# Optimization experiments

Hardware: AMD Instinct MI355X
Metric: run time of the kernel (lower is better)

## Reference

```python
import jax, jax.numpy as jnp
import numpy as np

B, T, D, H = 2, 2048, 1024, 16
DH = D // H

def setup_inputs() -> dict:
    key = jax.random.key(0)
    ks = jax.random.split(key, 5)
    scale = 1.0 / np.sqrt(D)
    x = jax.random.normal(ks[0], (B, T, D), dtype=jnp.float32)
    Wq = jax.random.normal(ks[1], (D, D), dtype=jnp.float32) * scale
    Wk = jax.random.normal(ks[2], (D, D), dtype=jnp.float32) * scale
    Wv = jax.random.normal(ks[3], (D, D), dtype=jnp.float32) * scale
    Wo = jax.random.normal(ks[4], (D, D), dtype=jnp.float32) * scale
    # causal mask: True means masked (matches torch masked_fill semantics)
    mask = jnp.triu(jnp.ones((T, T), dtype=bool), k=1)
    return {"x": x, "mask": mask, "Wq": Wq, "Wk": Wk, "Wv": Wv, "Wo": Wo}

def reference(x, mask, Wq, Wk, Wv, Wo):
    b, t, c = x.shape
    # projections -> [B, H, T, DH]
    def split_heads(y):
        return y.reshape(b, t, H, DH).transpose(0, 2, 1, 3)
    q = split_heads(x @ Wq)
    k = split_heads(x @ Wk)
    v = split_heads(x @ Wv)
    # scores [B, H, T, T]
    att = jnp.einsum('bhqd,bhkd->bhqk', q, k) / jnp.sqrt(jnp.float32(DH))
    att = jnp.where(mask, -jnp.inf, att)
    att = jax.nn.softmax(att, axis=-1)
    # dropout=0.0 (eval-mode determinism)
    out = jnp.einsum('bhqk,bhkd->bhqd', att, v)
    out = out.transpose(0, 2, 1, 3).reshape(b, t, c)
    return out @ Wo
```

## Files before the change

kernel.cpp:

```cpp
#include <hip/hip_runtime.h>
#include <stdint.h>

typedef unsigned short u16;
typedef unsigned int u32;
typedef __attribute__((ext_vector_type(8))) short s16x8;
typedef __attribute__((ext_vector_type(4))) float f32x4;
typedef __attribute__((ext_vector_type(8))) unsigned short u16x8;
typedef __attribute__((ext_vector_type(4))) unsigned short u16x4;

#define T_ 2048
#define D_ 1024
#define H_ 16
#define DH_ 64

#define QSCALE_LOG2E 0.18033688011112042f

#if __has_builtin(__builtin_amdgcn_exp2f)
#define EXP2(x) __builtin_amdgcn_exp2f(x)
#else
#define EXP2(x) exp2f(x)
#endif

__device__ __forceinline__ float bf2f(u16 u) {
    union { unsigned int i; float f; } x; x.i = ((unsigned int)u) << 16; return x.f;
}
__device__ __forceinline__ u16 f2bf(float f) {
    union { float f; unsigned int i; } x; x.f = f;
    unsigned int u = x.i;
    u += 0x7fffu + ((u >> 16) & 1u);
    return (u16)(u >> 16);
}
__device__ __forceinline__ u32 pack_rn(float a, float b) {
    union { float f; u32 u; } ua, ub; ua.f = a; ub.f = b;
    return ((ua.u + 0x8000u) >> 16) | ((ub.u + 0x8000u) & 0xffff0000u);
}

__device__ __forceinline__ void gload16(const u16* g, u16* l) {
    __builtin_amdgcn_global_load_lds(
        (const __attribute__((address_space(1))) void*)g,
        (__attribute__((address_space(3))) void*)l,
        16, 0, 0);
}

__global__ __launch_bounds__(256) void cvt_x_kernel(const float* __restrict__ x,
                                                    u16* __restrict__ xb) {
    int i = (blockIdx.x * 256 + threadIdx.x) * 4;
    float4 v = *(const float4*)(x + i);
    u16x4 o;
    o[0] = f2bf(v.x); o[1] = f2bf(v.y); o[2] = f2bf(v.z); o[3] = f2bf(v.w);
    *(u16x4*)(xb + i) = o;
}

__global__ __launch_bounds__(256) void transpose_w_kernel(const float* __restrict__ Wq,
                                                          const float* __restrict__ Wk,
                                                          const float* __restrict__ Wv,
                                                          const float* __restrict__ Wo,
                                                          u16* __restrict__ WT) {
    __shared__ float tile[32][33];
    int s = blockIdx.z;
    const float* W = (s == 0) ? Wq : (s == 1) ? Wk : (s == 2) ? Wv : Wo;
    int n0 = blockIdx.x * 32;
    int k0 = blockIdx.y * 32;
    int tx = threadIdx.x, ty = threadIdx.y;
    #pragma unroll
    for (int j = 0; j < 32; j += 8)
        tile[ty + j][tx] = W[(k0 + ty + j) * D_ + n0 + tx];
    __syncthreads();
    u16* dst = WT + (size_t)s * D_ * D_;
    #pragma unroll
    for (int j = 0; j < 32; j += 8)
        dst[(n0 + ty + j) * D_ + k0 + tx] = f2bf(tile[tx][ty + j]);
}

__global__ __launch_bounds__(256) void gemm_qkv(const u16* __restrict__ A,
                                                const u16* __restrict__ Bt,
                                                u16* __restrict__ Qw,
                                                u16* __restrict__ Kw,
                                                u16* __restrict__ Vw) {
    __shared__ __align__(16) u16 As[2][128 * 32];
    __shared__ __align__(16) u16 Bs[2][128 * 32];
    const int m0 = blockIdx.x * 128, n0 = blockIdx.y * 128;
    int tid = threadIdx.x;
    int w = tid >> 6, lane = tid & 63, quad = lane >> 4, l15 = lane & 15;
    int wr = w >> 1, wc = w & 1;

    int nb0 = (w << 7), nb1 = nb0 + 64;
    int c0 = nb0 + lane, c1 = nb1 + lane;
    int r0 = c0 >> 2, k0off = (c0 & 3) << 3;
    int r1 = c1 >> 2, k1off = (c1 & 3) << 3;
    const u16* Ar0 = A + (size_t)(m0 + r0) * D_ + k0off;
    const u16* Ar1 = A + (size_t)(m0 + r1) * D_ + k1off;
    const u16* Br0 = Bt + (size_t)(n0 + r0) * D_ + k0off;
    const u16* Br1 = Bt + (size_t)(n0 + r1) * D_ + k1off;

    f32x4 acc[4][4];
    #pragma unroll
    for (int mi = 0; mi < 4; ++mi)
        #pragma unroll
        for (int ni = 0; ni < 4; ++ni) acc[mi][ni] = (f32x4){0.f, 0.f, 0.f, 0.f};

    gload16(Ar0, &As[0][nb0 << 3]);
    gload16(Ar1, &As[0][nb1 << 3]);
    gload16(Br0, &Bs[0][nb0 << 3]);
    gload16(Br1, &Bs[0][nb1 << 3]);

    for (int k0 = 0; k0 < D_; k0 += 32) {
        int buf = (k0 >> 5) & 1;
        __syncthreads();
        if (k0 + 32 < D_) {
            int kn = k0 + 32;
            gload16(Ar0 + kn, &As[buf ^ 1][nb0 << 3]);
            gload16(Ar1 + kn, &As[buf ^ 1][nb1 << 3]);
            gload16(Br0 + kn, &Bs[buf ^ 1][nb0 << 3]);
            gload16(Br1 + kn, &Bs[buf ^ 1][nb1 << 3]);
        }
        s16x8 af[4], bf[4];
        #pragma unroll
        for (int mi = 0; mi < 4; ++mi)
            af[mi] = *(const s16x8*)&As[buf][((wr * 64 + mi * 16 + l15) << 5) + (quad << 3)];
        #pragma unroll
        for (int ni = 0; ni < 4; ++ni)
            bf[ni] = *(const s16x8*)&Bs[buf][((wc * 64 + ni * 16 + l15) << 5) + (quad << 3)];
        #pragma unroll
        for (int mi = 0; mi < 4; ++mi)
            #pragma unroll
            for (int ni = 0; ni < 4; ++ni)
                acc[mi][ni] = __builtin_amdgcn_mfma_f32_16x16x32_bf16(af[mi], bf[ni],
                                                                      acc[mi][ni], 0, 0, 0);
    }

    #pragma unroll
    for (int mi = 0; mi < 4; ++mi) {
        int mbase = m0 + wr * 64 + mi * 16 + quad * 4;
        #pragma unroll
        for (int ni = 0; ni < 4; ++ni) {
            int n = n0 + wc * 64 + ni * 16 + l15;
            int b = mbase >> 11, t0 = mbase & 2047;
            int sel = n >> 10, nn = n & 1023;
            int h = nn >> 6, dh = nn & 63;
            int bhidx = (b << 4) + h;
            if (sel == 0) {
                #pragma unroll
                for (int r = 0; r < 4; ++r)
                    Qw[(size_t)(bhidx * T_ + t0 + r) * DH_ + dh] =
                        f2bf(acc[mi][ni][r] * QSCALE_LOG2E);
            } else if (sel == 1) {
                #pragma unroll
                for (int r = 0; r < 4; ++r)
                    Kw[(size_t)(bhidx * T_ + t0 + r) * DH_ + dh] = f2bf(acc[mi][ni][r]);
            } else {
                uint2 pk;
                pk.x = pack_rn(acc[mi][ni][0], acc[mi][ni][1]);
                pk.y = pack_rn(acc[mi][ni][2], acc[mi][ni][3]);
                *(uint2*)(Vw + ((size_t)bhidx * DH_ + dh) * T_ + t0) = pk;
            }
        }
    }
}

__global__ __launch_bounds__(256) void gemm_out(const u16* __restrict__ A,
                                                const u16* __restrict__ Bt,
                                                float* __restrict__ Cout) {
    __shared__ __align__(16) u16 As[2][128 * 32];
    __shared__ __align__(16) u16 Bs[2][64 * 32];
    const int m0 = blockIdx.x * 128, n0 = blockIdx.y * 64;
    int tid = threadIdx.x;
    int w = tid >> 6, lane = tid & 63, quad = lane >> 4, l15 = lane & 15;

    int nbA0 = (w << 7), nbA1 = nbA0 + 64, nbB = (w << 6);
    int cA0 = nbA0 + lane, cA1 = nbA1 + lane, cB = nbB + lane;
    const u16* ArA0 = A + (size_t)(m0 + (cA0 >> 2)) * D_ + ((cA0 & 3) << 3);
    const u16* ArA1 = A + (size_t)(m0 + (cA1 >> 2)) * D_ + ((cA1 & 3) << 3);
    const u16* BrB  = Bt + (size_t)(n0 + (cB >> 2)) * D_ + ((cB & 3) << 3);

    f32x4 acc[2][4];
    #pragma unroll
    for (int mi = 0; mi < 2; ++mi)
        #pragma unroll
        for (int ni = 0; ni < 4; ++ni) acc[mi][ni] = (f32x4){0.f, 0.f, 0.f, 0.f};

    gload16(ArA0, &As[0][nbA0 << 3]);
    gload16(ArA1, &As[0][nbA1 << 3]);
    gload16(BrB,  &Bs[0][nbB << 3]);

    for (int k0 = 0; k0 < D_; k0 += 32) {
        int buf = (k0 >> 5) & 1;
        __syncthreads();
        if (k0 + 32 < D_) {
            int kn = k0 + 32;
            gload16(ArA0 + kn, &As[buf ^ 1][nbA0 << 3]);
            gload16(ArA1 + kn, &As[buf ^ 1][nbA1 << 3]);
            gload16(BrB + kn,  &Bs[buf ^ 1][nbB << 3]);
        }
        s16x8 af[2], bf[4];
        #pragma unroll
        for (int mi = 0; mi < 2; ++mi)
            af[mi] = *(const s16x8*)&As[buf][((w * 32 + mi * 16 + l15) << 5) + (quad << 3)];
        #pragma unroll
        for (int ni = 0; ni < 4; ++ni)
            bf[ni] = *(const s16x8*)&Bs[buf][((ni * 16 + l15) << 5) + (quad << 3)];
        #pragma unroll
        for (int mi = 0; mi < 2; ++mi)
            #pragma unroll
            for (int ni = 0; ni < 4; ++ni)
                acc[mi][ni] = __builtin_amdgcn_mfma_f32_16x16x32_bf16(af[mi], bf[ni],
                                                                      acc[mi][ni], 0, 0, 0);
    }

    #pragma unroll
    for (int mi = 0; mi < 2; ++mi) {
        int mbase = m0 + w * 32 + mi * 16 + quad * 4;
        #pragma unroll
        for (int ni = 0; ni < 4; ++ni) {
            int n = n0 + ni * 16 + l15;
            #pragma unroll
            for (int r = 0; r < 4; ++r)
                Cout[(size_t)(mbase + r) * D_ + n] = acc[mi][ni][r];
        }
    }
}

__global__ __launch_bounds__(256) void attn_mfma_kernel(const u16* __restrict__ Qg,
                                                        const u16* __restrict__ Kg,
                                                        const u16* __restrict__ Vt,
                                                        u16* __restrict__ att) {
    __shared__ __align__(16) u16 Kbuf[2][64 * 64];
    __shared__ __align__(16) u16 Vbuf[2][64 * 64];
    __shared__ __align__(16) u16 Ps[4][2][16][72];

    int bx = (int)gridDim.x - 1 - (int)blockIdx.x;
    int bh = blockIdx.y;
    int tid = threadIdx.x;
    int w = tid >> 6, lane = tid & 63, quad = lane >> 4, l15 = lane & 15;
    int q0 = bx * 128;
    int qA = q0 + 16 * w;
    int qB = q0 + 64 + 16 * w;

    const u16* Qb = Qg + (size_t)bh * T_ * DH_;
    const u16* Kb = Kg + (size_t)bh * T_ * DH_;
    const u16* Vb = Vt + (size_t)bh * DH_ * T_;

    s16x8 qa0 = *(const s16x8*)(Qb + (size_t)(qA + l15) * DH_ + quad * 8);
    s16x8 qa1 = *(const s16x8*)(Qb + (size_t)(qA + l15) * DH_ + quad * 8 + 32);
    s16x8 qc0 = *(const s16x8*)(Qb + (size_t)(qB + l15) * DH_ + quad * 8);
    s16x8 qc1 = *(const s16x8*)(Qb + (size_t)(qB + l15) * DH_ + quad * 8 + 32);

    int nb0 = (w << 7), nb1 = nb0 + 64;
    int n0c = nb0 + lane, n1c = nb1 + lane;
    int r0 = n0c >> 3, c0s = n0c & 7, g0 = (r0 << 3) + (c0s ^ (r0 & 7));
    int r1 = n1c >> 3, c1s = n1c & 7, g1 = (r1 << 3) + (c1s ^ (r1 & 7));

    gload16(Kb + (g0 << 3), &Kbuf[0][nb0 << 3]);
    gload16(Kb + (g1 << 3), &Kbuf[0][nb1 << 3]);
    gload16(Vb + (size_t)r0 * T_ + ((g0 & 7) << 3), &Vbuf[0][nb0 << 3]);
    gload16(Vb + (size_t)r1 * T_ + ((g1 & 7) << 3), &Vbuf[0][nb1 << 3]);

    f32x4 oA[4] = {{0.f,0.f,0.f,0.f},{0.f,0.f,0.f,0.f},{0.f,0.f,0.f,0.f},{0.f,0.f,0.f,0.f}};
    f32x4 oB[4] = {{0.f,0.f,0.f,0.f},{0.f,0.f,0.f,0.f},{0.f,0.f,0.f,0.f},{0.f,0.f,0.f,0.f}};
    float lA = 0.f, lB = 0.f;

    int ktmax = 2 * bx + 1;
    for (int kt = 0; kt <= ktmax; ++kt) {
        int buf = kt & 1;
        __syncthreads();

        if (kt < ktmax) {
            int kb2 = (kt + 1) << 6;
            const u16* Ktile = Kb + (size_t)kb2 * DH_;
            gload16(Ktile + (g0 << 3), &Kbuf[buf ^ 1][nb0 << 3]);
            gload16(Ktile + (g1 << 3), &Kbuf[buf ^ 1][nb1 << 3]);
            gload16(Vb + (size_t)r0 * T_ + kb2 + ((g0 & 7) << 3), &Vbuf[buf ^ 1][nb0 << 3]);
            gload16(Vb + (size_t)r1 * T_ + kb2 + ((g1 & 7) << 3), &Vbuf[buf ^ 1][nb1 << 3]);
        }

        f32x4 sA[4], sB[4];
        #pragma unroll
        for (int g = 0; g < 4; ++g) {
            int r = (g << 4) + l15;
            int cc = quad ^ (r & 7);
            s16x8 ka0 = *(const s16x8*)&Kbuf[buf][((r << 3) + cc) << 3];
            s16x8 ka1 = *(const s16x8*)&Kbuf[buf][((r << 3) + (cc ^ 4)) << 3];
            f32x4 z = {0.f, 0.f, 0.f, 0.f};
            sA[g] = __builtin_amdgcn_mfma_f32_16x16x32_bf16(ka0, qa0, z, 0, 0, 0);
            sA[g] = __builtin_amdgcn_mfma_f32_16x16x32_bf16(ka1, qa1, sA[g], 0, 0, 0);
            sB[g] = __builtin_amdgcn_mfma_f32_16x16x32_bf16(ka0, qc0, z, 0, 0, 0);
            sB[g] = __builtin_amdgcn_mfma_f32_16x16x32_bf16(ka1, qc1, sB[g], 0, 0, 0);
        }

        if (kt >= ktmax - 1) {
            int rA = q0 + 16 * w + l15 - (kt << 6);
            #pragma unroll
            for (int g = 0; g < 4; ++g)
                #pragma unroll
                for (int r = 0; r < 4; ++r)
                    if ((g << 4) + (quad << 2) + r > rA) sA[g][r] = -INFINITY;
        }
        if (kt == ktmax) {
            int rB = 16 * w + l15;
            #pragma unroll
            for (int g = 0; g < 4; ++g)
                #pragma unroll
                for (int r = 0; r < 4; ++r)
                    if ((g << 4) + (quad << 2) + r > rB) sB[g][r] = -INFINITY;
        }

        #pragma unroll
        for (int g = 0; g < 4; ++g)
            #pragma unroll
            for (int r = 0; r < 4; ++r) {
                float pA = EXP2(sA[g][r]); sA[g][r] = pA; lA += pA;
                float pB = EXP2(sB[g][r]); sB[g][r] = pB; lB += pB;
            }

        #pragma unroll
        for (int g = 0; g < 4; ++g) {
            uint2 pkA, pkB;
            pkA.x = pack_rn(sA[g][0], sA[g][1]); pkA.y = pack_rn(sA[g][2], sA[g][3]);
            pkB.x = pack_rn(sB[g][0], sB[g][1]); pkB.y = pack_rn(sB[g][2], sB[g][3]);
            *(uint2*)&Ps[w][0][l15][g * 16 + quad * 4] = pkA;
            *(uint2*)&Ps[w][1][l15][g * 16 + quad * 4] = pkB;
        }
        s16x8 pa0 = *(const s16x8*)&Ps[w][0][l15][quad * 8];
        s16x8 pa1 = *(const s16x8*)&Ps[w][0][l15][quad * 8 + 32];
        s16x8 pc0 = *(const s16x8*)&Ps[w][1][l15][quad * 8];
        s16x8 pc1 = *(const s16x8*)&Ps[w][1][l15][quad * 8 + 32];

        #pragma unroll
        for (int g = 0; g < 4; ++g) {
            int r = (g << 4) + l15;
            int cc = quad ^ (r & 7);
            s16x8 va0 = *(const s16x8*)&Vbuf[buf][((r << 3) + cc) << 3];
            s16x8 va1 = *(const s16x8*)&Vbuf[buf][((r << 3) + (cc ^ 4)) << 3];
            oA[g] = __builtin_amdgcn_mfma_f32_16x16x32_bf16(va0, pa0, oA[g], 0, 0, 0);
            oA[g] = __builtin_amdgcn_mfma_f32_16x16x32_bf16(va1, pa1, oA[g], 0, 0, 0);
            oB[g] = __builtin_amdgcn_mfma_f32_16x16x32_bf16(va0, pc0, oB[g], 0, 0, 0);
            oB[g] = __builtin_amdgcn_mfma_f32_16x16x32_bf16(va1, pc1, oB[g], 0, 0, 0);
        }
    }

    lA += __shfl_xor(lA, 16); lA += __shfl_xor(lA, 32);
    lB += __shfl_xor(lB, 16); lB += __shfl_xor(lB, 32);
    float invA = 1.f / lA, invB = 1.f / lB;
    int b = bh >> 4, h = bh & 15;
    u16* dstA = att + (size_t)(b * T_ + qA + l15) * D_ + (h << 6);
    u16* dstB = att + (size_t)(b * T_ + qB + l15) * D_ + (h << 6);
    #pragma unroll
    for (int g = 0; g < 4; ++g) {
        uint2 pk;
        pk.x = (u32)f2bf(oA[g][0] * invA) | ((u32)f2bf(oA[g][1] * invA) << 16);
        pk.y = (u32)f2bf(oA[g][2] * invA) | ((u32)f2bf(oA[g][3] * invA) << 16);
        *(uint2*)(dstA + (g << 4) + (quad << 2)) = pk;
        pk.x = (u32)f2bf(oB[g][0] * invB) | ((u32)f2bf(oB[g][1] * invB) << 16);
        pk.y = (u32)f2bf(oB[g][2] * invB) | ((u32)f2bf(oB[g][3] * invB) << 16);
        *(uint2*)(dstB + (g << 4) + (quad << 2)) = pk;
    }
}

extern "C" void kernel_launch(void* const* d_in, const int* in_sizes, int n_in,
                              void* d_out, int out_size, void* d_ws, size_t ws_size,
                              hipStream_t stream) {
    const float* x  = (const float*)d_in[0];
    const float* Wq = (const float*)d_in[2];
    const float* Wk = (const float*)d_in[3];
    const float* Wv = (const float*)d_in[4];
    const float* Wo = (const float*)d_in[5];
    float* out = (float*)d_out;

    char* ws = (char*)d_ws;
    u16* xb  = (u16*)(ws);
    u16* WT  = (u16*)(ws + (8ull  << 20));
    u16* Qw  = (u16*)(ws + (16ull << 20));
    u16* Kw  = (u16*)(ws + (24ull << 20));
    u16* Vw  = (u16*)(ws + (32ull << 20));
    u16* att = (u16*)(ws + (40ull << 20));

    cvt_x_kernel<<<dim3(4096), dim3(256), 0, stream>>>(x, xb);
    transpose_w_kernel<<<dim3(32, 32, 4), dim3(32, 8), 0, stream>>>(Wq, Wk, Wv, Wo, WT);
    gemm_qkv<<<dim3(32, 24), dim3(256), 0, stream>>>(xb, WT, Qw, Kw, Vw);
    attn_mfma_kernel<<<dim3(16, 32), dim3(256), 0, stream>>>(Qw, Kw, Vw, att);
    gemm_out<<<dim3(32, 16), dim3(256), 0, stream>>>(att, WT + 3ull * 1048576ull, out);
}
```

Baseline: 209.4 us.

## Split causal attention along KV into chunks and add a reduction kernel

The attention kernel now launches a flat 1280-block grid. Each block handles a 128-query tile and a chunk of up to 8 KV tiles, so long causal rows are spread across several blocks, and the grid is mapped so each XCD gets four heads. Partial unnormalized outputs (bf16) and row sums are written to workspace, and a new reduce kernel sums the chunks and normalizes. This targets load imbalance and low occupancy from the causal triangle, at the cost of an extra launch, extra global traffic, and bf16 rounding of the partials. Combining chunks without a running max is valid only because the kernel already skips max subtraction.

```diff
diff --git a/kernel.cpp b/kernel.cpp
--- a/kernel.cpp
+++ b/kernel.cpp
@@ -223,16 +223,28 @@
 __global__ __launch_bounds__(256) void attn_mfma_kernel(const u16* __restrict__ Qg,
                                                         const u16* __restrict__ Kg,
                                                         const u16* __restrict__ Vt,
-                                                        u16* __restrict__ att) {
+                                                        u16* __restrict__ Opart,
+                                                        float* __restrict__ lpart) {
     __shared__ __align__(16) u16 Kbuf[2][64 * 64];
     __shared__ __align__(16) u16 Vbuf[2][64 * 64];
     __shared__ __align__(16) u16 Ps[4][2][16][72];
 
-    int bx = (int)gridDim.x - 1 - (int)blockIdx.x;
-    int bh = blockIdx.y;
+    int blk = blockIdx.x;
+    int xcd = blk & 7, slot = blk >> 3;
+    int bh = (xcd << 2) + (slot / 40);
+    int x  = slot % 40;
+    int BX, c;
+    if (x < 4)       { BX = x;                    c = 0; }
+    else if (x < 12) { BX = 4 + ((x - 4) >> 1);   c = (x - 4) & 1; }
+    else if (x < 24) { BX = 8 + (x - 12) / 3;     c = (x - 12) % 3; }
+    else             { BX = 12 + ((x - 24) >> 2); c = (x - 24) & 3; }
+    int kstart = c << 3;
+    int ktm = 2 * BX + 1;
+    int kend = min(kstart + 8, ktm + 1);
+
     int tid = threadIdx.x;
     int w = tid >> 6, lane = tid & 63, quad = lane >> 4, l15 = lane & 15;
-    int q0 = bx * 128;
+    int q0 = BX << 7;
     int qA = q0 + 16 * w;
     int qB = q0 + 64 + 16 * w;
 
@@ -250,21 +262,24 @@
     int r0 = n0c >> 3, c0s = n0c & 7, g0 = (r0 << 3) + (c0s ^ (r0 & 7));
     int r1 = n1c >> 3, c1s = n1c & 7, g1 = (r1 << 3) + (c1s ^ (r1 & 7));
 
-    gload16(Kb + (g0 << 3), &Kbuf[0][nb0 << 3]);
-    gload16(Kb + (g1 << 3), &Kbuf[0][nb1 << 3]);
-    gload16(Vb + (size_t)r0 * T_ + ((g0 & 7) << 3), &Vbuf[0][nb0 << 3]);
-    gload16(Vb + (size_t)r1 * T_ + ((g1 & 7) << 3), &Vbuf[0][nb1 << 3]);
+    {
+        int kb0 = kstart << 6;
+        const u16* Ktile = Kb + (size_t)kb0 * DH_;
+        gload16(Ktile + (g0 << 3), &Kbuf[0][nb0 << 3]);
+        gload16(Ktile + (g1 << 3), &Kbuf[0][nb1 << 3]);
+        gload16(Vb + (size_t)r0 * T_ + kb0 + ((g0 & 7) << 3), &Vbuf[0][nb0 << 3]);
+        gload16(Vb + (size_t)r1 * T_ + kb0 + ((g1 & 7) << 3), &Vbuf[0][nb1 << 3]);
+    }
 
     f32x4 oA[4] = {{0.f,0.f,0.f,0.f},{0.f,0.f,0.f,0.f},{0.f,0.f,0.f,0.f},{0.f,0.f,0.f,0.f}};
     f32x4 oB[4] = {{0.f,0.f,0.f,0.f},{0.f,0.f,0.f,0.f},{0.f,0.f,0.f,0.f},{0.f,0.f,0.f,0.f}};
     float lA = 0.f, lB = 0.f;
 
-    int ktmax = 2 * bx + 1;
-    for (int kt = 0; kt <= ktmax; ++kt) {
-        int buf = kt & 1;
+    for (int kt = kstart; kt < kend; ++kt) {
+        int buf = (kt - kstart) & 1;
         __syncthreads();
 
-        if (kt < ktmax) {
+        if (kt + 1 < kend) {
             int kb2 = (kt + 1) << 6;
             const u16* Ktile = Kb + (size_t)kb2 * DH_;
             gload16(Ktile + (g0 << 3), &Kbuf[buf ^ 1][nb0 << 3]);
@@ -287,7 +302,7 @@
             sB[g] = __builtin_amdgcn_mfma_f32_16x16x32_bf16(ka1, qc1, sB[g], 0, 0, 0);
         }
 
-        if (kt >= ktmax - 1) {
+        if (kt >= ktm - 1) {
             int rA = q0 + 16 * w + l15 - (kt << 6);
             #pragma unroll
             for (int g = 0; g < 4; ++g)
@@ -295,7 +310,7 @@
                 for (int r = 0; r < 4; ++r)
                     if ((g << 4) + (quad << 2) + r > rA) sA[g][r] = -INFINITY;
         }
-        if (kt == ktmax) {
+        if (kt == ktm) {
             int rB = 16 * w + l15;
             #pragma unroll
             for (int g = 0; g < 4; ++g)
@@ -340,19 +355,63 @@
 
     lA += __shfl_xor(lA, 16); lA += __shfl_xor(lA, 32);
     lB += __shfl_xor(lB, 16); lB += __shfl_xor(lB, 32);
-    float invA = 1.f / lA, invB = 1.f / lB;
-    int b = bh >> 4, h = bh & 15;
-    u16* dstA = att + (size_t)(b * T_ + qA + l15) * D_ + (h << 6);
-    u16* dstB = att + (size_t)(b * T_ + qB + l15) * D_ + (h << 6);
+    int slotid = ((bh << 4) + BX) * 4 + c;
+    u16* dA = Opart + ((size_t)slotid * 128 + 16 * w + l15) * 64;
+    u16* dB = dA + 64 * 64;
     #pragma unroll
     for (int g = 0; g < 4; ++g) {
         uint2 pk;
-        pk.x = (u32)f2bf(oA[g][0] * invA) | ((u32)f2bf(oA[g][1] * invA) << 16);
-        pk.y = (u32)f2bf(oA[g][2] * invA) | ((u32)f2bf(oA[g][3] * invA) << 16);
-        *(uint2*)(dstA + (g << 4) + (quad << 2)) = pk;
-        pk.x = (u32)f2bf(oB[g][0] * invB) | ((u32)f2bf(oB[g][1] * invB) << 16);
-        pk.y = (u32)f2bf(oB[g][2] * invB) | ((u32)f2bf(oB[g][3] * invB) << 16);
-        *(uint2*)(dstB + (g << 4) + (quad << 2)) = pk;
+        pk.x = pack_rn(oA[g][0], oA[g][1]); pk.y = pack_rn(oA[g][2], oA[g][3]);
+        *(uint2*)(dA + (g << 4) + (quad << 2)) = pk;
+        pk.x = pack_rn(oB[g][0], oB[g][1]); pk.y = pack_rn(oB[g][2], oB[g][3]);
+        *(uint2*)(dB + (g << 4) + (quad << 2)) = pk;
+    }
+    if (quad == 0) {
+        lpart[(size_t)slotid * 128 + 16 * w + l15] = lA;
+        lpart[(size_t)slotid * 128 + 64 + 16 * w + l15] = lB;
+    }
+}
+
+__global__ __launch_bounds__(256) void reduce_attn(const u16* __restrict__ Opart,
+                                                   const float* __restrict__ lpart,
+                                                   u16* __restrict__ att) {
+    int BX = blockIdx.x, bh = blockIdx.y;
+    int nch = (BX >> 2) + 1;
+    int tid = threadIdx.x;
+    int row = tid >> 1, dh0 = (tid & 1) << 5;
+    int slotbase = ((bh << 4) + BX) << 2;
+
+    float acc[32];
+    #pragma unroll
+    for (int i = 0; i < 32; ++i) acc[i] = 0.f;
+    float l = 0.f;
+    for (int cc = 0; cc < nch; ++cc) {
+        const u16* op = Opart + ((size_t)(slotbase + cc) * 128 + row) * 64 + dh0;
+        #pragma unroll
+        for (int v = 0; v < 4; ++v) {
+            u16x8 o8 = *(const u16x8*)(op + v * 8);
+            #pragma unroll
+            for (int j = 0; j < 8; ++j) acc[v * 8 + j] += bf2f(o8[j]);
+        }
+        l += lpart[(size_t)(slotbase + cc) * 128 + row];
+    }
+    float inv = 1.f / l;
+    int b = bh >> 4, h = bh & 15;
+    int q = (BX << 7) + row;
+    u16* dst = att + ((size_t)(b * T_) + q) * D_ + (h << 6) + dh0;
+    #pragma unroll
+    for (int v = 0; v < 2; ++v) {
+        u16x8 o8;
+        #pragma unroll
+        for (int j = 0; j < 8; ++j) o8[j] = f2bf(acc[v * 16 + j * 2] * inv),
+                                    o8[j] = o8[j];
+        #pragma unroll
+        for (int j = 0; j < 8; ++j) o8[j] = f2bf(acc[v * 16 + j] * inv);
+        u16x8 o8b;
+        #pragma unroll
+        for (int j = 0; j < 8; ++j) o8b[j] = f2bf(acc[v * 16 + 8 + j] * inv);
+        *(u16x8*)(dst + v * 16) = o8;
+        *(u16x8*)(dst + v * 16 + 8) = o8b;
     }
 }
 
@@ -367,16 +426,19 @@
     float* out = (float*)d_out;
 
     char* ws = (char*)d_ws;
-    u16* xb  = (u16*)(ws);
-    u16* WT  = (u16*)(ws + (8ull  << 20));
-    u16* Qw  = (u16*)(ws + (16ull << 20));
-    u16* Kw  = (u16*)(ws + (24ull << 20));
-    u16* Vw  = (u16*)(ws + (32ull << 20));
-    u16* att = (u16*)(ws + (40ull << 20));
+    u16*   xb    = (u16*)(ws);
+    u16*   WT    = (u16*)(ws + (8ull  << 20));
+    u16*   Qw    = (u16*)(ws + (16ull << 20));
+    u16*   Kw    = (u16*)(ws + (24ull << 20));
+    u16*   Vw    = (u16*)(ws + (32ull << 20));
+    u16*   att   = (u16*)(ws + (40ull << 20));
+    u16*   Opart = (u16*)(ws + (48ull << 20));
+    float* lpart = (float*)(ws + (82ull << 20));
 
     cvt_x_kernel<<<dim3(4096), dim3(256), 0, stream>>>(x, xb);
     transpose_w_kernel<<<dim3(32, 32, 4), dim3(32, 8), 0, stream>>>(Wq, Wk, Wv, Wo, WT);
     gemm_qkv<<<dim3(32, 24), dim3(256), 0, stream>>>(xb, WT, Qw, Kw, Vw);
-    attn_mfma_kernel<<<dim3(16, 32), dim3(256), 0, stream>>>(Qw, Kw, Vw, att);
+    attn_mfma_kernel<<<dim3(1280), dim3(256), 0, stream>>>(Qw, Kw, Vw, Opart, lpart);
+    reduce_attn<<<dim3(16, 32), dim3(256), 0, stream>>>(Opart, lpart, att);
     gemm_out<<<dim3(32, 16), dim3(256), 0, stream>>>(att, WT + 3ull * 1048576ull, out);
 }
```

Result: faster. 200.0 us (-4.5%).
